# Performance work log

Measured on AMD Instinct MI355X. Metric: run time of the kernel, lower is better.

The kernel has to match this reference:

```python
import jax, jax.numpy as jnp
import numpy as np

GRID = 64
AABB_MIN = np.array([-1.25, -1.55, -1.25], dtype=np.float32)
AABB_MAX = np.array([1.25, 0.95, 1.25], dtype=np.float32)
DENSITY_THRESH = 0.5


def setup_inputs() -> dict:
    key = jax.random.key(0)
    ks = jax.random.split(key, 12)
    N, S, H = 8192, 128, 64
    rays_o = jax.random.normal(ks[0], (N, 3), jnp.float32) * 0.1
    d = jax.random.normal(ks[1], (N, 3), jnp.float32)
    rays_d = d / jnp.sqrt(jnp.clip(jnp.sum(d * d, -1, keepdims=True), 1e-20))
    near = 0.05 + jax.random.uniform(ks[2], (N,), jnp.float32) * 0.5
    far = near + 2.0 + jax.random.uniform(ks[3], (N,), jnp.float32) * 0.5
    jitter = jax.random.uniform(ks[4], (N, S), jnp.float32)
    density_field = jax.random.uniform(ks[5], (GRID, GRID, GRID), jnp.float32)
    W1 = jax.random.normal(ks[6], (3, H), jnp.float32) * 0.5
    b1 = jnp.zeros((H,), jnp.float32)
    W2 = jax.random.normal(ks[7], (H, H), jnp.float32) * (1.0 / np.sqrt(H))
    b2 = jnp.zeros((H,), jnp.float32)
    Wsig = jax.random.normal(ks[8], (H, 1), jnp.float32) * (1.0 / np.sqrt(H))
    bsig = jnp.zeros((1,), jnp.float32)
    Wrgb = jax.random.normal(ks[9], (H, 3), jnp.float32) * (1.0 / np.sqrt(H))
    brgb = jnp.zeros((3,), jnp.float32)
    return {"rays_o": rays_o, "rays_d": rays_d, "near": near, "far": far,
            "jitter": jitter, "density_field": density_field,
            "W1": W1, "b1": b1, "W2": W2, "b2": b2,
            "Wsig": Wsig, "bsig": bsig, "Wrgb": Wrgb, "brgb": brgb}


def _render_train(rays_o, rays_d, near, far, jitter, density_field,
                  W1, b1, W2, b2, Wsig, bsig, Wrgb, brgb):
    N, S = jitter.shape
    step = (far - near) / S                                  # [N]
    offset = jnp.asarray(AABB_MIN)
    scale = jnp.asarray(AABB_MAX) - jnp.asarray(AABB_MIN)
    # uniform march (raymarch_train): z_i = near + i*step, zeroed where grid empty
    z = near[:, None] + jnp.arange(S, dtype=jnp.float32)[None, :] * step[:, None]  # [N,S]
    pts0 = rays_o[:, None, :] + z[..., None] * rays_d[:, None, :]                  # [N,S,3]
    u = (pts0 - offset) / scale
    idx = jnp.floor(u * GRID).astype(jnp.int32)
    inb = jnp.all((idx >= 0) & (idx < GRID), axis=-1)
    idxc = jnp.clip(idx, 0, GRID - 1)
    occ = density_field[idxc[..., 0], idxc[..., 1], idxc[..., 2]] > DENSITY_THRESH
    z_vals = jnp.where(occ & inb, z, 0.0)                    # [N,S]
    mask = z_vals > 0
    # stratified jitter (torch: z_vals + rand * step_size)
    z_vals = z_vals + jitter * step[:, None]
    pts = rays_o[:, None, :] + z_vals[..., None] * rays_d[:, None, :]  # [N,S,3]
    # radiance-field MLP (stand-in for `model(pts, None)`)
    h = jax.nn.relu(jnp.einsum('nsc,ch->nsh', pts, W1) + b1)
    h = jax.nn.relu(jnp.einsum('nsh,hk->nsk', h, W2) + b2)
    sigma = (jnp.einsum('nsh,ho->nso', h, Wsig) + bsig)[..., 0]        # [N,S]
    rgb = jax.nn.sigmoid(jnp.einsum('nsh,ho->nso', h, Wrgb) + brgb)    # [N,S,3]
    # torch fills masked-out samples with sigma=-1000, rgb=0
    sigma = jnp.where(mask, sigma, -1000.0)
    rgb = jnp.where(mask[..., None], rgb, 0.0)
    # composite
    dists = jnp.broadcast_to(step[:, None], sigma.shape)
    tau = jax.nn.relu(sigma) * dists
    alpha = 1.0 - jnp.exp(-tau)
    trans = jnp.concatenate([jnp.ones_like(alpha[..., :1]),
                             jnp.cumprod(1.0 - alpha + 1e-10, axis=-1)], axis=-1)
    w = alpha * trans[..., :-1]                              # [N,S]
    no_hit = trans[..., -1]
    color = jnp.sum(w[..., None] * rgb, axis=-2) + no_hit[..., None]   # bg_color=None -> white
    depth = jnp.sum(w * z_vals, axis=-1)
    return color, depth


def reference(rays_o, rays_d, near, far, jitter, density_field,
              W1, b1, W2, b2, Wsig, bsig, Wrgb, brgb):
    color, depth = _render_train(rays_o, rays_d, near, far, jitter, density_field,
                                 W1, b1, W2, b2, Wsig, bsig, Wrgb, brgb)
    return color
```

## Files before the change

kernel.cpp:

```cpp
#include <hip/hip_runtime.h>
#include <math.h>

#define S 128
#define H 64
#define RPB 8
#define SPB (RPB * S)
#define T 256

typedef __attribute__((ext_vector_type(8))) short bf16x8;
typedef __attribute__((ext_vector_type(4))) short short4s;
typedef __attribute__((ext_vector_type(4))) float f32x4;
typedef __attribute__((ext_vector_type(2))) unsigned int u32x2;
#define MFMA16(a, b, c) __builtin_amdgcn_mfma_f32_16x16x32_bf16((a), (b), (c), 0, 0, 0)

__device__ __forceinline__ short f2bf(float x) {
    __bf16 b = (__bf16)x;
    return __builtin_bit_cast(short, b);
}

__device__ __forceinline__ unsigned lds_off(const void* p) {
    return (unsigned)(size_t)p;
}

union frag_u { bf16x8 v; u32x2 d[2]; };

__device__ __forceinline__ void tr_load_pair(unsigned addr, bf16x8& f0, bf16x8& f1) {
    u32x2 r0, r1, r2, r3;
    asm volatile(
        "ds_read_b64_tr_b16 %0, %4 offset:0\n\t"
        "ds_read_b64_tr_b16 %1, %4 offset:128\n\t"
        "ds_read_b64_tr_b16 %2, %4 offset:1024\n\t"
        "ds_read_b64_tr_b16 %3, %4 offset:1152\n\t"
        "s_waitcnt lgkmcnt(0)"
        : "=v"(r0), "=v"(r1), "=v"(r2), "=v"(r3)
        : "v"(addr) : "memory");
    frag_u u0; u0.d[0] = r0; u0.d[1] = r1; f0 = u0.v;
    frag_u u1; u1.d[0] = r2; u1.d[1] = r3; f1 = u1.v;
}

__device__ __forceinline__ bool sample_mask(
    float ox, float oy, float oz, float dx, float dy, float dz,
    float nr, float step, int s, const float* __restrict__ density)
{
    const float z  = __fadd_rn(nr, __fmul_rn((float)s, step));
    const float px = __fadd_rn(ox, __fmul_rn(z, dx));
    const float py = __fadd_rn(oy, __fmul_rn(z, dy));
    const float pz = __fadd_rn(oz, __fmul_rn(z, dz));
    const float gx = floorf(__fmul_rn(__fdiv_rn(__fsub_rn(px, -1.25f), 2.5f), 64.0f));
    const float gy = floorf(__fmul_rn(__fdiv_rn(__fsub_rn(py, -1.55f), 2.5f), 64.0f));
    const float gz = floorf(__fmul_rn(__fdiv_rn(__fsub_rn(pz, -1.25f), 2.5f), 64.0f));
    const int ix = (int)gx, iy = (int)gy, iz = (int)gz;
    const bool inb = (ix >= 0) && (ix < 64) && (iy >= 0) && (iy < 64) &&
                     (iz >= 0) && (iz < 64);
    const int cx = min(max(ix, 0), 63);
    const int cy = min(max(iy, 0), 63);
    const int cz = min(max(iz, 0), 63);
    const float dval = density[(cx << 12) | (cy << 6) | cz];
    return inb && (dval > 0.5f);
}

__global__ __launch_bounds__(256, 5)
void fused_mfma_kernel(const float* __restrict__ rays_o, const float* __restrict__ rays_d,
                       const float* __restrict__ nearv, const float* __restrict__ farv,
                       const float* __restrict__ jitter, const float* __restrict__ density,
                       const float* __restrict__ W1, const float* __restrict__ b1,
                       const float* __restrict__ W2, const float* __restrict__ b2,
                       const float* __restrict__ Wsig, const float* __restrict__ bsig,
                       const float* __restrict__ Wrgb, const float* __restrict__ brgb,
                       float* __restrict__ out, int N)
{
    __shared__ __align__(16) union {
        short w2t[H * 72];
        float rg[2 * SPB];
    } s_u;
    __shared__ __align__(128) short hT[4][H * 16];
    __shared__ unsigned short s_list[SPB];
    __shared__ __align__(16) float s_alpha[SPB];
    __shared__ __align__(16) float s_bv[SPB];
    __shared__ __align__(16) float s_ray[RPB][8];
    __shared__ int s_wcnt[4];
    __shared__ int s_wbase[4];

    short* const sW2t = s_u.w2t;
    float* const s_r  = s_u.rg;
    float* const s_g  = s_u.rg + SPB;
    float* const s_b  = s_bv;

    const int tid  = threadIdx.x;
    const int lane = tid & 63;
    const int wv   = tid >> 6;
    const int blk  = blockIdx.x;
    const int mrow = lane & 15;
    const int quad = lane >> 4;

    if (tid < RPB) {
        const int gr = blk * RPB + tid;
        float ox = 0.f, oy = 0.f, oz = 0.f, dx = 0.f, dy = 0.f, dz = 0.f,
              nr = 0.f, st = 0.f;
        if (gr < N) {
            ox = rays_o[gr * 3 + 0]; oy = rays_o[gr * 3 + 1]; oz = rays_o[gr * 3 + 2];
            dx = rays_d[gr * 3 + 0]; dy = rays_d[gr * 3 + 1]; dz = rays_d[gr * 3 + 2];
            nr = nearv[gr];
            st = __fdiv_rn(__fsub_rn(farv[gr], nr), 128.0f);
        }
        s_ray[tid][0] = ox; s_ray[tid][1] = oy; s_ray[tid][2] = oz; s_ray[tid][3] = dx;
        s_ray[tid][4] = dy; s_ray[tid][5] = dz; s_ray[tid][6] = nr; s_ray[tid][7] = st;
    }
    for (int e = tid; e < H * H; e += T) {
        const int k = e >> 6, n = e & 63;
        sW2t[n * 72 + k] = f2bf(W2[e]);
    }
    __syncthreads();

    const int lbase = tid * 4;
    const int rloc  = lbase >> 7;
    const int gra   = blk * RPB + rloc;
    unsigned int mybits = 0u;
    {
        const float4 rv0 = *reinterpret_cast<const float4*>(&s_ray[rloc][0]);
        const float4 rv1 = *reinterpret_cast<const float4*>(&s_ray[rloc][4]);
        if (gra < N) {
            const int s0 = lbase & (S - 1);
            #pragma unroll
            for (int j = 0; j < 4; ++j) {
                if (sample_mask(rv0.x, rv0.y, rv0.z, rv0.w, rv1.x, rv1.y,
                                rv1.z, rv1.w, s0 + j, density))
                    mybits |= (1u << j);
            }
        }
    }
    const int mycnt = __popc(mybits);
    int inc = mycnt;
    #pragma unroll
    for (int off = 1; off < 64; off <<= 1) {
        const int u = __shfl_up(inc, off, 64);
        if (lane >= off) inc += u;
    }
    if (lane == 63) s_wcnt[wv] = inc;

    bf16x8 w2f[4][2];
    #pragma unroll
    for (int nt = 0; nt < 4; ++nt) {
        #pragma unroll
        for (int ks = 0; ks < 2; ++ks) {
            w2f[nt][ks] = *(const bf16x8*)&sW2t[(mrow + 16 * nt) * 72 + 32 * ks + 8 * quad];
        }
    }
    bf16x8 w1f[4];
    #pragma unroll
    for (int nt = 0; nt < 4; ++nt) {
        bf16x8 f = {0, 0, 0, 0, 0, 0, 0, 0};
        if (quad == 0) {
            const int n = mrow + 16 * nt;
            f[0] = f2bf(W1[n]);
            f[1] = f2bf(W1[64 + n]);
            f[2] = f2bf(W1[128 + n]);
            f[3] = f2bf(b1[n]);
        }
        w1f[nt] = f;
    }
    bf16x8 a3f[2];
    #pragma unroll
    for (int ks = 0; ks < 2; ++ks) {
        bf16x8 f = {0, 0, 0, 0, 0, 0, 0, 0};
        if (mrow < 4) {
            #pragma unroll
            for (int j = 0; j < 8; ++j) {
                const int k = 32 * ks + 8 * quad + j;
                const float v = (mrow == 0) ? Wsig[k] : Wrgb[k * 3 + (mrow - 1)];
                f[j] = f2bf(v);
            }
        }
        a3f[ks] = f;
    }
    float b2v[4];
    #pragma unroll
    for (int nt = 0; nt < 4; ++nt) b2v[nt] = b2[mrow + 16 * nt];
    const float bsg = bsig[0];
    const float br0 = brgb[0], br1 = brgb[1], br2 = brgb[2];

    __syncthreads();
    if (tid == 0) {
        int t0 = 0;
        #pragma unroll
        for (int i = 0; i < 4; ++i) { s_wbase[i] = t0; t0 += s_wcnt[i]; }
    }
    __syncthreads();
    int pos = s_wbase[wv] + (inc - mycnt);
    #pragma unroll
    for (int j = 0; j < 4; ++j) {
        if ((mybits >> j) & 1u) {
            s_list[pos++] = (unsigned short)(lbase + j);
        } else {
            s_alpha[lbase + j] = 0.0f;
            s_r[lbase + j] = 0.0f;
            s_g[lbase + j] = 0.0f;
            s_b[lbase + j] = 0.0f;
        }
    }
    const int K = s_wbase[3] + s_wcnt[3];
    __syncthreads();

    const f32x4 z4 = {0.f, 0.f, 0.f, 0.f};
    const int ntask = (K + 15) >> 4;
    short* const hb2 = &hT[wv][0];
    short4s* const hst = (short4s*)&hb2[mrow * 16 + 4 * quad];
    const unsigned trA = lds_off(hb2) + 8 * mrow + 256 * quad;

    int nid = 0, nval = 0;
    float njit = 0.0f;
    if (ntask > wv) {
        const int slot = (wv << 4) + mrow;
        nval = slot < K;
        nid = s_list[nval ? slot : 0];
        njit = jitter[blk * SPB + nid];
    }

    for (int t = wv; t < ntask; t += 4) {
        const int id = nid;
        const int valid = nval;
        const float jit = njit;
        const int tn = t + 4;
        if (tn < ntask) {
            const int slot = (tn << 4) + mrow;
            nval = slot < K;
            nid = s_list[nval ? slot : 0];
            njit = jitter[blk * SPB + nid];
        }

        const int ri = id >> 7;
        const int s  = id & (S - 1);
        const float4 rv0 = *reinterpret_cast<const float4*>(&s_ray[ri][0]);
        const float4 rv1 = *reinterpret_cast<const float4*>(&s_ray[ri][4]);
        const float nr = rv1.z, step = rv1.w;
        const float zs = __fadd_rn(nr, __fmul_rn((float)s, step));
        const float zj = zs + jit * step;
        const float qx = rv0.x + zj * rv0.w;
        const float qy = rv0.y + zj * rv1.x;
        const float qz = rv0.z + zj * rv1.y;

        bf16x8 ah = {0, 0, 0, 0, 0, 0, 0, 0};
        if (quad == 0) {
            ah[0] = f2bf(qx); ah[1] = f2bf(qy); ah[2] = f2bf(qz);
            ah[3] = (short)0x3F80;
        }
        #pragma unroll
        for (int nt = 0; nt < 4; ++nt) {
            const f32x4 c1 = MFMA16(ah, w1f[nt], z4);
            short4s pk;
            pk[0] = f2bf(fmaxf(c1[0], 0.0f));
            pk[1] = f2bf(fmaxf(c1[1], 0.0f));
            pk[2] = f2bf(fmaxf(c1[2], 0.0f));
            pk[3] = f2bf(fmaxf(c1[3], 0.0f));
            hst[nt * 64] = pk;
        }

        bf16x8 a2_0, a2_1;
        tr_load_pair(trA, a2_0, a2_1);
        #pragma unroll
        for (int nt = 0; nt < 4; ++nt) {
            const f32x4 c2 = MFMA16(a2_1, w2f[nt][1], MFMA16(a2_0, w2f[nt][0], z4));
            short4s pk;
            pk[0] = f2bf(fmaxf(c2[0] + b2v[nt], 0.0f));
            pk[1] = f2bf(fmaxf(c2[1] + b2v[nt], 0.0f));
            pk[2] = f2bf(fmaxf(c2[2] + b2v[nt], 0.0f));
            pk[3] = f2bf(fmaxf(c2[3] + b2v[nt], 0.0f));
            hst[nt * 64] = pk;
        }

        bf16x8 b3_0, b3_1;
        tr_load_pair(trA, b3_0, b3_1);
        const f32x4 c3 = MFMA16(a3f[1], b3_1, MFMA16(a3f[0], b3_0, z4));

        if (quad == 0 && valid) {
            const float sg = c3[0] + bsg;
            const float tau = fmaxf(sg, 0.0f) * step;
            s_alpha[id] = 1.0f - __expf(-tau);
            s_r[id] = __builtin_amdgcn_rcpf(1.0f + __expf(-(c3[1] + br0)));
            s_g[id] = __builtin_amdgcn_rcpf(1.0f + __expf(-(c3[2] + br1)));
            s_b[id] = __builtin_amdgcn_rcpf(1.0f + __expf(-(c3[3] + br2)));
        }
    }
    __syncthreads();

    #pragma unroll
    for (int ri = wv; ri < RPB; ri += 4) {
        const int gr = blk * RPB + ri;
        if (gr >= N) break;
        const int b0 = ri * S + 2 * lane;
        const float2 a01 = *reinterpret_cast<const float2*>(&s_alpha[b0]);
        const float a0 = a01.x, a1 = a01.y;
        const float t0 = (1.0f - a0) + 1e-10f;
        const float t1 = (1.0f - a1) + 1e-10f;
        float v = t0 * t1;
        #pragma unroll
        for (int off = 1; off < 64; off <<= 1) {
            const float u = __shfl_up(v, off, 64);
            if (lane >= off) v *= u;
        }
        float excl = __shfl_up(v, 1, 64);
        if (lane == 0) excl = 1.0f;
        const float no_hit = __shfl(v, 63, 64);
        const float w0 = a0 * excl;
        const float w1 = a1 * (excl * t0);
        const float2 r01 = *reinterpret_cast<const float2*>(&s_r[b0]);
        const float2 g01 = *reinterpret_cast<const float2*>(&s_g[b0]);
        const float2 b01 = *reinterpret_cast<const float2*>(&s_b[b0]);
        float cr = w0 * r01.x + w1 * r01.y;
        float cg = w0 * g01.x + w1 * g01.y;
        float cb = w0 * b01.x + w1 * b01.y;
        #pragma unroll
        for (int off = 32; off >= 1; off >>= 1) {
            cr += __shfl_xor(cr, off, 64);
            cg += __shfl_xor(cg, off, 64);
            cb += __shfl_xor(cb, off, 64);
        }
        if (lane == 0) {
            out[gr * 3 + 0] = cr + no_hit;
            out[gr * 3 + 1] = cg + no_hit;
            out[gr * 3 + 2] = cb + no_hit;
        }
    }
}

extern "C" void kernel_launch(void* const* d_in, const int* in_sizes, int n_in,
                              void* d_out, int out_size, void* d_ws, size_t ws_size,
                              hipStream_t stream) {
    const float* rays_o  = (const float*)d_in[0];
    const float* rays_d  = (const float*)d_in[1];
    const float* nearv   = (const float*)d_in[2];
    const float* farv    = (const float*)d_in[3];
    const float* jitter  = (const float*)d_in[4];
    const float* density = (const float*)d_in[5];
    const float* W1      = (const float*)d_in[6];
    const float* b1      = (const float*)d_in[7];
    const float* W2      = (const float*)d_in[8];
    const float* b2      = (const float*)d_in[9];
    const float* Wsig    = (const float*)d_in[10];
    const float* bsig    = (const float*)d_in[11];
    const float* Wrgb    = (const float*)d_in[12];
    const float* brgb    = (const float*)d_in[13];
    float* out = (float*)d_out;

    const int N = in_sizes[2];

    fused_mfma_kernel<<<dim3((N + RPB - 1) / RPB), dim3(T), 0, stream>>>(
        rays_o, rays_d, nearv, farv, jitter, density,
        W1, b1, W2, b2, Wsig, bsig, Wrgb, brgb, out, N);
}
```

Baseline: 100.3 us.

## Halve rays per block, compact samples via LDS atomic, vectorize W2 load

Each block now handles 4 rays instead of 8, so each thread tests 2 samples and each wavefront owns exactly one ray. The per-wave prefix bases come from an LDS atomicAdd instead of a serial tid-0 scan, which drops one barrier. The W2 transpose into LDS now uses float4 global loads. The grid doubles in block count, so the per-block W2 staging and weight-fragment setup is repeated twice as often in exchange for more parallelism. The compacted sample order across waves is no longer deterministic.

Result: slower. 106.3 us (+6.0%).

```diff
diff --git a/kernel.cpp b/kernel.cpp
--- a/kernel.cpp
+++ b/kernel.cpp
@@ -3,7 +3,7 @@
 
 #define S 128
 #define H 64
-#define RPB 8
+#define RPB 4
 #define SPB (RPB * S)
 #define T 256
 
@@ -78,8 +78,7 @@
     __shared__ __align__(16) float s_alpha[SPB];
     __shared__ __align__(16) float s_bv[SPB];
     __shared__ __align__(16) float s_ray[RPB][8];
-    __shared__ int s_wcnt[4];
-    __shared__ int s_wbase[4];
+    __shared__ int s_total;
 
     short* const sW2t = s_u.w2t;
     float* const s_r  = s_u.rg;
@@ -93,6 +92,7 @@
     const int mrow = lane & 15;
     const int quad = lane >> 4;
 
+    if (tid == 0) s_total = 0;
     if (tid < RPB) {
         const int gr = blk * RPB + tid;
         float ox = 0.f, oy = 0.f, oz = 0.f, dx = 0.f, dy = 0.f, dz = 0.f,
@@ -106,23 +106,29 @@
         s_ray[tid][0] = ox; s_ray[tid][1] = oy; s_ray[tid][2] = oz; s_ray[tid][3] = dx;
         s_ray[tid][4] = dy; s_ray[tid][5] = dz; s_ray[tid][6] = nr; s_ray[tid][7] = st;
     }
-    for (int e = tid; e < H * H; e += T) {
+    #pragma unroll
+    for (int e4 = tid; e4 < (H * H) / 4; e4 += T) {
+        const float4 w = reinterpret_cast<const float4*>(W2)[e4];
+        const int e = e4 * 4;
         const int k = e >> 6, n = e & 63;
-        sW2t[n * 72 + k] = f2bf(W2[e]);
+        sW2t[(n + 0) * 72 + k] = f2bf(w.x);
+        sW2t[(n + 1) * 72 + k] = f2bf(w.y);
+        sW2t[(n + 2) * 72 + k] = f2bf(w.z);
+        sW2t[(n + 3) * 72 + k] = f2bf(w.w);
     }
     __syncthreads();
 
-    const int lbase = tid * 4;
-    const int rloc  = lbase >> 7;
+    const int lbase = tid * 2;
+    const int rloc  = wv;
     const int gra   = blk * RPB + rloc;
     unsigned int mybits = 0u;
     {
         const float4 rv0 = *reinterpret_cast<const float4*>(&s_ray[rloc][0]);
         const float4 rv1 = *reinterpret_cast<const float4*>(&s_ray[rloc][4]);
         if (gra < N) {
-            const int s0 = lbase & (S - 1);
+            const int s0 = 2 * lane;
             #pragma unroll
-            for (int j = 0; j < 4; ++j) {
+            for (int j = 0; j < 2; ++j) {
                 if (sample_mask(rv0.x, rv0.y, rv0.z, rv0.w, rv1.x, rv1.y,
                                 rv1.z, rv1.w, s0 + j, density))
                     mybits |= (1u << j);
@@ -136,7 +142,9 @@
         const int u = __shfl_up(inc, off, 64);
         if (lane >= off) inc += u;
     }
-    if (lane == 63) s_wcnt[wv] = inc;
+    int wbase0 = 0;
+    if (lane == 63) wbase0 = atomicAdd(&s_total, inc);
+    const int wbase = __shfl(wbase0, 63, 64);
 
     bf16x8 w2f[4][2];
     #pragma unroll
@@ -180,15 +188,11 @@
     const float br0 = brgb[0], br1 = brgb[1], br2 = brgb[2];
 
     __syncthreads();
-    if (tid == 0) {
-        int t0 = 0;
-        #pragma unroll
-        for (int i = 0; i < 4; ++i) { s_wbase[i] = t0; t0 += s_wcnt[i]; }
-    }
-    __syncthreads();
-    int pos = s_wbase[wv] + (inc - mycnt);
-    #pragma unroll
-    for (int j = 0; j < 4; ++j) {
+    const int K = s_total;
+
+    int pos = wbase + (inc - mycnt);
+    #pragma unroll
+    for (int j = 0; j < 2; ++j) {
         if ((mybits >> j) & 1u) {
             s_list[pos++] = (unsigned short)(lbase + j);
         } else {
@@ -198,7 +202,6 @@
             s_b[lbase + j] = 0.0f;
         }
     }
-    const int K = s_wbase[3] + s_wcnt[3];
     __syncthreads();
 
     const f32x4 z4 = {0.f, 0.f, 0.f, 0.f};
```
